# Kernel optimization log

Hardware: AMD Instinct MI355X
Metric: run time of the kernel (lower is better)

## Reference

```python
import jax, jax.numpy as jnp
import numpy as np

A = 16          # n_agents
H = 128         # rnn_hidden_dim
IN = 128        # input_shape
NA = 32         # n_attention
NACT = 14       # n_actions
TAU = 0.5       # gumbel_softmax_tau
B_ENV = 1024    # parallel envs
BZ = B_ENV * A

# neighbor index: for agent i, all j != i (matches select_ind in torch code)
IDX = np.array([[j for j in range(A) if j != i] for i in range(A)])  # [A, A-1]


def gru_cell(x, h, Wih, Whh, bih, bhh):
    # torch GRUCell gate order: r, z, n
    gi = x @ Wih.T + bih
    gh = h @ Whh.T + bhh
    ir, iz, inn = jnp.split(gi, 3, axis=-1)
    hr, hz, hn = jnp.split(gh, 3, axis=-1)
    r = jax.nn.sigmoid(ir + hr)
    z = jax.nn.sigmoid(iz + hz)
    n = jnp.tanh(inn + r * hn)
    return (1.0 - z) * n + z * h


def run_gru(seq, Wih, Whh, bih, bhh):
    # seq: [T, N, D]; returns all hidden states [T, N, H]
    h0 = jnp.zeros((seq.shape[1], Whh.shape[1]), seq.dtype)
    def step(h, x):
        h2 = gru_cell(x, h, Wih, Whh, bih, bhh)
        return h2, h2
    _, ys = jax.lax.scan(step, h0, seq)
    return ys


def setup_inputs() -> dict:
    key = jax.random.key(0)
    ks = jax.random.split(key, 24)
    def u(k, shape, fan):
        s = 1.0 / np.sqrt(fan)
        return jax.random.uniform(k, shape, jnp.float32, -s, s)
    inp = {
        "inputs": jax.random.normal(ks[0], (BZ, IN), jnp.float32),
        "hidden_state": jax.random.normal(ks[1], (BZ, H), jnp.float32),
        "gumbel_u": jax.random.uniform(ks[2], (BZ * (A - 1), 2), jnp.float32),
        # fc1
        "W1": u(ks[3], (H, IN), IN), "b1": u(ks[4], (H,), IN),
        # GRUCell
        "Wih_c": u(ks[5], (3 * H, H), H), "Whh_c": u(ks[6], (3 * H, H), H),
        "bih_c": u(ks[7], (3 * H,), H), "bhh_c": u(ks[8], (3 * H,), H),
        # bi-GRU forward dir (input 2H)
        "Wih_f": u(ks[9], (3 * H, 2 * H), H), "Whh_f": u(ks[10], (3 * H, H), H),
        "bih_f": u(ks[11], (3 * H,), H), "bhh_f": u(ks[12], (3 * H,), H),
        # bi-GRU backward dir
        "Wih_b": u(ks[13], (3 * H, 2 * H), H), "Whh_b": u(ks[14], (3 * H, H), H),
        "bih_b": u(ks[15], (3 * H,), H), "bhh_b": u(ks[16], (3 * H,), H),
        # hard classifier
        "Wc": u(ks[17], (2, 2 * H), 2 * H), "bc": u(ks[18], (2,), 2 * H),
        # attention projections (no bias)
        "Wq": u(ks[19], (NA, H), H), "Wk": u(ks[20], (NA, H), H),
        # fc2
        "W2": u(ks[21], (NACT, 2 * H), 2 * H), "b2": u(ks[22], (NACT,), 2 * H),
    }
    return inp


def reference(inputs, hidden_state, gumbel_u, W1, b1, Wih_c, Whh_c, bih_c, bhh_c,
              Wih_f, Whh_f, bih_f, bhh_f, Wih_b, Whh_b, bih_b, bhh_b,
              Wc, bc, Wq, Wk, W2, b2):
    bz = inputs.shape[0]
    B = bz // A
    x1 = jax.nn.relu(inputs @ W1.T + b1)
    h_rnn = gru_cell(x1, hidden_state.reshape(-1, H), Wih_c, Whh_c, bih_c, bhh_c)  # [bz, H]

    h3 = h_rnn.reshape(B, A, H)
    nbr = h3[:, IDX, :]                                           # [B, A, A-1, H]
    self_rep = jnp.broadcast_to(h3[:, :, None, :], (B, A, A - 1, H))
    pairs = jnp.concatenate([self_rep, nbr], axis=-1)             # [B, A, A-1, 2H]
    seq = pairs.transpose(2, 0, 1, 3).reshape(A - 1, bz, 2 * H)   # [T, bz, 2H]

    yf = run_gru(seq, Wih_f, Whh_f, bih_f, bhh_f)
    yb = jnp.flip(run_gru(jnp.flip(seq, 0), Wih_b, Whh_b, bih_b, bhh_b), 0)
    h_hard = jnp.concatenate([yf, yb], axis=-1)                   # [T, bz, 2H]
    h_hard = h_hard.transpose(1, 0, 2).reshape(-1, 2 * H)         # [bz*T, 2H]

    logits = h_hard @ Wc.T + bc                                   # [bz*T, 2]
    g = -jnp.log(-jnp.log(gumbel_u + 1e-10) + 1e-10)
    gs = jax.nn.softmax((logits + g) / TAU, axis=-1)
    hard_w = gs[:, 1].reshape(B, A, A - 1)                        # hard gate

    q = (h_rnn @ Wq.T).reshape(B, A, NA)
    k = (h_rnn @ Wk.T).reshape(B, A, NA)
    kn = k[:, IDX, :] * hard_w[..., None]                         # [B, A, A-1, NA]
    scores = jnp.einsum('bad,bamd->bam', q, kn) / np.sqrt(NA)
    soft_w = jax.nn.softmax(scores, axis=-1)                      # [B, A, A-1]

    w = hard_w * soft_w
    agg = jnp.einsum('bam,bamh->bah', w, nbr).reshape(bz, H)
    out = jnp.concatenate([h_rnn, agg], axis=-1) @ W2.T + b2      # [bz, n_actions]
    return out, h_rnn
```

## Files before the change

### kernel.cpp

```cpp
#include <hip/hip_runtime.h>
#include <hip/hip_bf16.h>


typedef __attribute__((ext_vector_type(8))) short short8;
typedef __attribute__((ext_vector_type(4))) short short4v;
typedef __attribute__((ext_vector_type(4))) float float4v;

#define BF2F(x) __bfloat162float(x)
typedef __hip_bfloat16 bf;

__device__ __forceinline__ float frcp(float x) {
  return __builtin_amdgcn_rcpf(x);
}
__device__ __forceinline__ float fsigmoid(float x) {
  return frcp(1.f + __expf(-x));
}
__device__ __forceinline__ float ftanh(float x) {
  float e = __expf(2.f * x);
  return 1.f - 2.f * frcp(1.f + e);
}
__device__ __forceinline__ float rdv(const void* p, int i, int f) {
  return f ? ((const float*)p)[i] : BF2F(((const bf*)p)[i]);
}

static const int AO[23] = {
  0, 2097152, 4194304, 4685824, 4702208, 4702336, 4751488, 4800640, 4801024,
  4801408, 4899712, 4948864, 4949248, 4949632, 5047936, 5097088, 5097472,
  5097856, 5098368, 5098384, 5102480, 5106576, 5110160};
static const int AN[23] = {
  2097152, 2097152, 491520, 16384, 128, 49152, 49152, 384, 384, 98304, 49152,
  384, 384, 98304, 49152, 384, 384, 512, 2, 4096, 4096, 3584, 14};

struct CArgs {
  const void* src[23];
  int n[23];
  int off[23];
};

__global__ void kConvert(CArgs a, int* __restrict__ flagOut,
                         bf* __restrict__ arena,
                         const void* __restrict__ WqR, const void* __restrict__ WkR,
                         const void* __restrict__ W2R, const void* __restrict__ WcR,
                         bf* __restrict__ Wqk, bf* __restrict__ W2p,
                         bf* __restrict__ Wcb) {
  __shared__ int sflag;
  if (threadIdx.x == 0) sflag = 0;
  __syncthreads();
  {
    const unsigned short* p0 = (const unsigned short*)a.src[0];
    int hit = 0;
    for (int i = threadIdx.x; i < 4096; i += 256) {
      int e = (p0[i] >> 7) & 0xFF;
      if (e >= 0xC0) hit = 1;
    }
    if (hit) atomicOr(&sflag, 1);
  }
  __syncthreads();
  const int f = sflag;
  const int b = blockIdx.y;
  if (b == 0 && blockIdx.x == 0 && threadIdx.x == 0) *flagOut = f;

  if (b == 23) {
    int idx = blockIdx.x * 256 + threadIdx.x;
    if (idx < 8192) {
      int r = idx >> 7, c = idx & 127;
      float v = (r < 32) ? rdv(WqR, r * 128 + c, f) : rdv(WkR, (r - 32) * 128 + c, f);
      Wqk[idx] = __float2bfloat16(v);
    }
    if (idx < 4096)
      W2p[idx] = __float2bfloat16((idx < 3584) ? rdv(W2R, idx, f) : 0.f);
    if (idx < 512) {
      int dir = idx >> 8, l = (idx >> 7) & 1, k = idx & 127;
      Wcb[idx] = __float2bfloat16(rdv(WcR, l * 256 + dir * 128 + k, f));
    }
    return;
  }
  if (b == 2 || b == 18 || b == 22) return;
  const int n = a.n[b];
  const int nv = n & ~7;
  bf* dst = arena + a.off[b];
  const int gid = blockIdx.x * 256 + threadIdx.x;
  const int gs = gridDim.x * 256;
  if (f) {
    const float* s = (const float*)a.src[b];
    for (int i = gid * 8; i < nv; i += gs * 8) {
      float4 x0 = *(const float4*)(s + i);
      float4 x1 = *(const float4*)(s + i + 4);
      short8 v;
      bf t;
      t = __float2bfloat16(x0.x); v[0] = *(short*)&t;
      t = __float2bfloat16(x0.y); v[1] = *(short*)&t;
      t = __float2bfloat16(x0.z); v[2] = *(short*)&t;
      t = __float2bfloat16(x0.w); v[3] = *(short*)&t;
      t = __float2bfloat16(x1.x); v[4] = *(short*)&t;
      t = __float2bfloat16(x1.y); v[5] = *(short*)&t;
      t = __float2bfloat16(x1.z); v[6] = *(short*)&t;
      t = __float2bfloat16(x1.w); v[7] = *(short*)&t;
      *(short8*)(dst + i) = v;
    }
    for (int i = nv + gid; i < n; i += gs) dst[i] = __float2bfloat16(s[i]);
  } else {
    const short8* s = (const short8*)a.src[b];
    short8* d = (short8*)dst;
    for (int i = gid; i * 8 < nv; i += gs) d[i] = s[i];
    const unsigned short* ss = (const unsigned short*)a.src[b];
    unsigned short* ds = (unsigned short*)dst;
    for (int i = nv + gid; i < n; i += gs) ds[i] = ss[i];
  }
}

__global__ __launch_bounds__(256) void kFused12(
    const bf* __restrict__ inputs, const bf* __restrict__ W1,
    const bf* __restrict__ b1, const bf* __restrict__ Wih,
    const bf* __restrict__ bih, bf* __restrict__ gi) {
  __shared__ bf sX[4][16][136];
  const int tid = threadIdx.x;
  const int wave = tid >> 6, lane = tid & 63;
  const int quad = lane >> 4, ci = lane & 15;
  const int row0 = blockIdx.x * 64 + wave * 16;

  float4v xa[8];
#pragma unroll
  for (int i = 0; i < 8; ++i) xa[i] = {0.f, 0.f, 0.f, 0.f};
#pragma unroll
  for (int ks = 0; ks < 4; ++ks) {
    short8 inr = *(const short8*)(inputs + (size_t)(row0 + ci) * 128 + ks * 32 + quad * 8);
#pragma unroll
    for (int ct = 0; ct < 8; ++ct) {
      short8 wfr = *(const short8*)(W1 + (size_t)(ct * 16 + ci) * 128 + ks * 32 + quad * 8);
      xa[ct] = __builtin_amdgcn_mfma_f32_16x16x32_bf16(wfr, inr, xa[ct], 0, 0, 0);
    }
  }
#pragma unroll
  for (int ct = 0; ct < 8; ++ct) {
    short4v v4;
#pragma unroll
    for (int r = 0; r < 4; ++r) {
      float v = xa[ct][r] + BF2F(b1[ct * 16 + quad * 4 + r]);
      v = fmaxf(v, 0.f);
      bf t = __float2bfloat16(v);
      v4[r] = *(short*)&t;
    }
    *(short4v*)&sX[wave][ci][ct * 16 + quad * 4] = v4;
  }
  short8 af[4];
#pragma unroll
  for (int ks = 0; ks < 4; ++ks)
    af[ks] = *(const short8*)&sX[wave][ci][ks * 32 + quad * 8];

  for (int cg = 0; cg < 6; ++cg) {
    float4v acc[4];
#pragma unroll
    for (int i = 0; i < 4; ++i) acc[i] = {0.f, 0.f, 0.f, 0.f};
#pragma unroll
    for (int ks = 0; ks < 4; ++ks)
#pragma unroll
      for (int nt = 0; nt < 4; ++nt) {
        short8 b = *(const short8*)(Wih + (size_t)(cg * 64 + nt * 16 + ci) * 128 + ks * 32 + quad * 8);
        acc[nt] = __builtin_amdgcn_mfma_f32_16x16x32_bf16(af[ks], b, acc[nt], 0, 0, 0);
      }
#pragma unroll
    for (int nt = 0; nt < 4; ++nt) {
      int col = cg * 64 + nt * 16 + ci;
      float bv = BF2F(bih[col]);
#pragma unroll
      for (int r = 0; r < 4; ++r)
        gi[(size_t)(row0 + quad * 4 + r) * 384 + col] = __float2bfloat16(acc[nt][r] + bv);
    }
  }
}

__global__ __launch_bounds__(256, 4) void kStep(
    const bf* __restrict__ Hp, const bf* __restrict__ Whh,
    const bf* __restrict__ G, int gld,
    const bf* __restrict__ bhh,
    bf* __restrict__ Ho, float* __restrict__ HcopyF) {
  const int half = blockIdx.z;
  const int tid = threadIdx.x;
  const int wave = tid >> 6, lane = tid & 63;
  const int quad = lane >> 4, ci = lane & 15;
  const int mr = blockIdx.x * 64 + wave * 16;

  float4v acc[12];
#pragma unroll
  for (int i = 0; i < 12; ++i) acc[i] = {0.f, 0.f, 0.f, 0.f};

#pragma unroll
  for (int ks = 0; ks < 4; ++ks) {
    short8 a = *(const short8*)(Hp + (size_t)(mr + ci) * 128 + ks * 32 + quad * 8);
#pragma unroll
    for (int g = 0; g < 3; ++g)
#pragma unroll
      for (int nt = 0; nt < 4; ++nt) {
        short8 b = *(const short8*)(Whh + (size_t)(g * 128 + half * 64 + nt * 16 + ci) * 128 + ks * 32 + quad * 8);
        acc[g * 4 + nt] = __builtin_amdgcn_mfma_f32_16x16x32_bf16(a, b, acc[g * 4 + nt], 0, 0, 0);
      }
  }

  float bR[4], bZ[4], bN[4];
#pragma unroll
  for (int nt = 0; nt < 4; ++nt) {
    int c = half * 64 + nt * 16 + ci;
    bR[nt] = BF2F(bhh[c]);
    bZ[nt] = BF2F(bhh[128 + c]);
    bN[nt] = BF2F(bhh[256 + c]);
  }

#pragma unroll
  for (int r = 0; r < 4; ++r) {
    int rr = mr + quad * 4 + r;
    const bf* gs = G + (size_t)rr * gld;
#pragma unroll
    for (int nt = 0; nt < 4; ++nt) {
      int c = half * 64 + nt * 16 + ci;
      float gr = BF2F(gs[c]), gz = BF2F(gs[128 + c]), gnn = BF2F(gs[256 + c]);
      float pre_r = acc[nt][r] + gr + bR[nt];
      float pre_z = acc[4 + nt][r] + gz + bZ[nt];
      float hn_   = acc[8 + nt][r] + bN[nt];
      float rg = fsigmoid(pre_r);
      float zg = fsigmoid(pre_z);
      float ng = ftanh(gnn + rg * hn_);
      float hp = BF2F(Hp[(size_t)rr * 128 + c]);
      float hv = ng + zg * (hp - ng);
      Ho[(size_t)rr * 128 + c] = __float2bfloat16(hv);
      if (HcopyF) HcopyF[(size_t)rr * 128 + c] = hv;
    }
  }
}

__global__ __launch_bounds__(512, 4) void kSeq(
    const bf* __restrict__ hrnn,
    const bf* __restrict__ Wih_f, const bf* __restrict__ Wih_b,
    const bf* __restrict__ Whh_f, const bf* __restrict__ Whh_b,
    const bf* __restrict__ bih_f, const bf* __restrict__ bih_b,
    const bf* __restrict__ bhh_f, const bf* __restrict__ bhh_b,
    const bf* __restrict__ Wcb, float* __restrict__ L) {
  __shared__ float sGiN[16][3][132];
  __shared__ bf sH[2][16][136];
  __shared__ float sL[16][15][2];
  __shared__ bf sWc[2][136];

  const int env = blockIdx.x;
  const int dir = blockIdx.y;
  const int tid = threadIdx.x;
  const int wave = tid >> 6, lane = tid & 63;
  const int nh = wave;
  const int quad = lane >> 4, ci = lane & 15;
  const bf* Wih = dir ? Wih_b : Wih_f;
  const bf* Whh = dir ? Whh_b : Whh_f;
  const bf* bih = dir ? bih_b : bih_f;
  const bf* bhh = dir ? bhh_b : bhh_f;
  const int h0q = nh * 16 + quad * 4;

  float4v gS[3], gN[3];
#pragma unroll
  for (int i = 0; i < 3; ++i) { gS[i] = {0.f, 0.f, 0.f, 0.f}; gN[i] = {0.f, 0.f, 0.f, 0.f}; }
#pragma unroll
  for (int ks = 0; ks < 4; ++ks) {
    short8 bh = *(const short8*)(hrnn + (size_t)(env * 16 + ci) * 128 + ks * 32 + quad * 8);
#pragma unroll
    for (int g = 0; g < 3; ++g) {
      const bf* wrow = Wih + (size_t)(g * 128 + nh * 16 + ci) * 256 + ks * 32 + quad * 8;
      short8 ws = *(const short8*)(wrow);
      short8 wn = *(const short8*)(wrow + 128);
      gS[g] = __builtin_amdgcn_mfma_f32_16x16x32_bf16(ws, bh, gS[g], 0, 0, 0);
      gN[g] = __builtin_amdgcn_mfma_f32_16x16x32_bf16(wn, bh, gN[g], 0, 0, 0);
    }
  }
#pragma unroll
  for (int g = 0; g < 3; ++g)
#pragma unroll
    for (int r = 0; r < 4; ++r) {
      int c = g * 128 + h0q + r;
      float bv = BF2F(bih[c]);
      if (g < 2) bv += BF2F(bhh[c]);
      gS[g][r] += bv;
    }
#pragma unroll
  for (int g = 0; g < 3; ++g)
    *(float4v*)&sGiN[ci][g][h0q] = gN[g];

  {
    bf z = __float2bfloat16(0.f);
    bf* p = &sH[0][0][0];
    for (int i = tid; i < 16 * 136; i += 512) p[i] = z;
    if (tid < 256)
      sWc[tid >> 7][tid & 127] = Wcb[(dir * 2 + (tid >> 7)) * 128 + (tid & 127)];
  }

  short8 Bf[12];
#pragma unroll
  for (int g = 0; g < 3; ++g)
#pragma unroll
    for (int ks = 0; ks < 4; ++ks)
      Bf[g * 4 + ks] =
          *(const short8*)(Whh + (size_t)(g * 128 + nh * 16 + ci) * 128 + ks * 32 + quad * 8);

  float bNc[4];
#pragma unroll
  for (int r = 0; r < 4; ++r) bNc[r] = BF2F(bhh[256 + h0q + r]);

  float hPrev[4];
#pragma unroll
  for (int r = 0; r < 4; ++r) hPrev[r] = 0.f;

  __syncthreads();

  for (int t = 0; t < 15; ++t) {
    const int cur = t & 1, nxt = cur ^ 1;
    const int m = dir ? (14 - t) : t;
    const int jr = m + ((m >= ci) ? 1 : 0);

    float4v nbR = *(const float4v*)&sGiN[jr][0][h0q];
    float4v nbZ = *(const float4v*)&sGiN[jr][1][h0q];
    float4v nbN = *(const float4v*)&sGiN[jr][2][h0q];

    float4v acc[3];
#pragma unroll
    for (int i = 0; i < 3; ++i) acc[i] = {0.f, 0.f, 0.f, 0.f};
    float4v lacc = {0.f, 0.f, 0.f, 0.f};
#pragma unroll
    for (int ks = 0; ks < 4; ++ks) {
      short8 bh = *(const short8*)&sH[cur][ci][ks * 32 + quad * 8];
#pragma unroll
      for (int g = 0; g < 3; ++g)
        acc[g] = __builtin_amdgcn_mfma_f32_16x16x32_bf16(Bf[g * 4 + ks], bh, acc[g], 0, 0, 0);
      if (nh == 0) {
        short8 wv = *(const short8*)&sWc[ci & 1][ks * 32 + quad * 8];
        lacc = __builtin_amdgcn_mfma_f32_16x16x32_bf16(wv, bh, lacc, 0, 0, 0);
      }
    }
    if (nh == 0 && t > 0 && quad == 0) {
      int mp = dir ? (15 - t) : (t - 1);
      sL[ci][mp][0] = lacc[0];
      sL[ci][mp][1] = lacc[1];
    }

    short4v hv4;
#pragma unroll
    for (int r = 0; r < 4; ++r) {
      float pre_r = acc[0][r] + gS[0][r] + nbR[r];
      float pre_z = acc[1][r] + gS[1][r] + nbZ[r];
      float gnn   = gS[2][r] + nbN[r];
      float hn_   = acc[2][r] + bNc[r];
      float rg = fsigmoid(pre_r);
      float zg = fsigmoid(pre_z);
      float ng = ftanh(gnn + rg * hn_);
      float hv = ng + zg * (hPrev[r] - ng);
      hPrev[r] = hv;
      bf b = __float2bfloat16(hv);
      hv4[r] = *(short*)&b;
    }
    *(short4v*)&sH[nxt][ci][h0q] = hv4;
    __syncthreads();
  }

  if (nh == 0) {
    float4v lacc = {0.f, 0.f, 0.f, 0.f};
#pragma unroll
    for (int ks = 0; ks < 4; ++ks) {
      short8 bh = *(const short8*)&sH[1][ci][ks * 32 + quad * 8];
      short8 wv = *(const short8*)&sWc[ci & 1][ks * 32 + quad * 8];
      lacc = __builtin_amdgcn_mfma_f32_16x16x32_bf16(wv, bh, lacc, 0, 0, 0);
    }
    if (quad == 0) {
      int mf = dir ? 0 : 14;
      sL[ci][mf][0] = lacc[0];
      sL[ci][mf][1] = lacc[1];
    }
  }
  __syncthreads();

  {
    float* Ld = L + (size_t)dir * 491520 + (size_t)env * 480;
    for (int i = tid; i < 480; i += 512) {
      int row = i / 30, rem = i - row * 30;
      int mm = rem >> 1, l = rem & 1;
      Ld[i] = sL[row][mm][l];
    }
  }
}

__global__ __launch_bounds__(256) void kTail(
    const bf* __restrict__ h, const bf* __restrict__ Wqk,
    const float* __restrict__ L, const void* __restrict__ guRaw,
    const void* __restrict__ bcRaw, const int* __restrict__ flag,
    const bf* __restrict__ W2p, const void* __restrict__ b2Raw,
    float* __restrict__ out) {
  __shared__ float sh[16 * 132];
  __shared__ float sqk[16 * 64];
  __shared__ float shw[240];
  __shared__ float sw[16 * 16];
  __shared__ bf sAgg[64][136];
  const int b4 = blockIdx.x;
  const int tid = threadIdx.x;
  const int f = *flag;
  const int a = tid >> 4, i = tid & 15;

  for (int e = 0; e < 4; ++e) {
    const int bb = b4 * 4 + e;
    __syncthreads();
    {
      const int w = tid >> 6, lane = tid & 63;
      const int quad = lane >> 4, ci = lane & 15;
      float4v acc = {0.f, 0.f, 0.f, 0.f};
#pragma unroll
      for (int ks = 0; ks < 4; ++ks) {
        short8 a_ = *(const short8*)(h + (size_t)(bb * 16 + ci) * 128 + ks * 32 + quad * 8);
        short8 b_ = *(const short8*)(Wqk + (size_t)(w * 16 + ci) * 128 + ks * 32 + quad * 8);
        acc = __builtin_amdgcn_mfma_f32_16x16x32_bf16(a_, b_, acc, 0, 0, 0);
      }
#pragma unroll
      for (int r = 0; r < 4; ++r)
        sqk[(quad * 4 + r) * 64 + w * 16 + ci] = acc[r];
    }
    for (int k = tid; k < 2048; k += 256)
      sh[(k >> 7) * 132 + (k & 127)] = BF2F(h[(size_t)bb * 2048 + k]);
    if (tid < 240) {
      int idx = bb * 240 + tid;
      float l0 = L[(size_t)idx * 2]     + L[491520 + (size_t)idx * 2]     + rdv(bcRaw, 0, f);
      float l1 = L[(size_t)idx * 2 + 1] + L[491520 + (size_t)idx * 2 + 1] + rdv(bcRaw, 1, f);
      float u0 = rdv(guRaw, idx * 2, f);
      float u1 = rdv(guRaw, idx * 2 + 1, f);
      float g0 = -__logf(-__logf(u0 + 1e-10f) + 1e-10f);
      float g1 = -__logf(-__logf(u1 + 1e-10f) + 1e-10f);
      shw[tid] = fsigmoid(((l1 + g1) - (l0 + g0)) * 2.0f);
    }
    __syncthreads();

    float s = -1e30f;
    if (i < 15) {
      int j = i + (i >= a);
      float d = 0.f;
#pragma unroll
      for (int c = 0; c < 32; ++c) d += sqk[a * 64 + c] * sqk[j * 64 + 32 + c];
      s = shw[a * 15 + i] * d * 0.17677669529663687f;
    }
    float mx = s;
#pragma unroll
    for (int d = 1; d < 16; d <<= 1) mx = fmaxf(mx, __shfl_xor(mx, d));
    float ex = (i < 15) ? __expf(s - mx) : 0.f;
    float sum = ex;
#pragma unroll
    for (int d = 1; d < 16; d <<= 1) sum += __shfl_xor(sum, d);
    float w = (i < 15) ? (ex * frcp(sum)) * shw[a * 15 + i] : 0.f;
    sw[a * 16 + i] = w;
    __syncthreads();

    float ac[8] = {0, 0, 0, 0, 0, 0, 0, 0};
    for (int mm = 0; mm < 15; ++mm) {
      int jm = mm + (mm >= a);
      float wm = sw[a * 16 + mm];
      const float* shp = &sh[jm * 132 + i * 8];
      float4 h0 = *(const float4*)shp;
      float4 h1 = *(const float4*)(shp + 4);
      ac[0] += wm * h0.x; ac[1] += wm * h0.y; ac[2] += wm * h0.z; ac[3] += wm * h0.w;
      ac[4] += wm * h1.x; ac[5] += wm * h1.y; ac[6] += wm * h1.z; ac[7] += wm * h1.w;
    }
    short8 v;
#pragma unroll
    for (int d = 0; d < 8; ++d) {
      bf b = __float2bfloat16(ac[d]);
      v[d] = *(short*)&b;
    }
    *(short8*)&sAgg[e * 16 + a][i * 8] = v;
  }
  __syncthreads();

  {
    const int wave = tid >> 6, lane = tid & 63;
    const int quad = lane >> 4, ci = lane & 15;
    const int mr = b4 * 64 + wave * 16;
    float4v acc = {0.f, 0.f, 0.f, 0.f};
#pragma unroll
    for (int ks = 0; ks < 4; ++ks) {
      short8 a_ = *(const short8*)(h + (size_t)(mr + ci) * 128 + ks * 32 + quad * 8);
      short8 b_ = *(const short8*)(W2p + (size_t)ci * 256 + ks * 32 + quad * 8);
      acc = __builtin_amdgcn_mfma_f32_16x16x32_bf16(a_, b_, acc, 0, 0, 0);
    }
#pragma unroll
    for (int ks = 0; ks < 4; ++ks) {
      short8 a_ = *(const short8*)&sAgg[wave * 16 + ci][ks * 32 + quad * 8];
      short8 b_ = *(const short8*)(W2p + (size_t)ci * 256 + 128 + ks * 32 + quad * 8);
      acc = __builtin_amdgcn_mfma_f32_16x16x32_bf16(a_, b_, acc, 0, 0, 0);
    }
    if (ci < 14) {
      float bv = rdv(b2Raw, ci, f);
#pragma unroll
      for (int r = 0; r < 4; ++r)
        out[(size_t)(mr + quad * 4 + r) * 14 + ci] = acc[r] + bv;
    }
  }
}

extern "C" void kernel_launch(void* const* d_in, const int* in_sizes, int n_in,
                              void* d_out, int out_size, void* d_ws, size_t ws_size,
                              hipStream_t stream) {
  const size_t OFF_ARENA = 0;
  const size_t OFF_FLAG  = 10220544;
  const size_t OFF_A     = 10220800;
  const size_t OFF_WQK   = 26998016;
  const size_t OFF_WCB   = 27014400;
  const size_t OFF_W2P   = 27410944;
  const size_t OFF_HRNN  = 27419136;
  const size_t NEEDED    = 84042240;
  if (ws_size < NEEDED) return;
  if (n_in < 23 || in_sizes[0] != 2097152 || in_sizes[3] != 16384 ||
      in_sizes[5] != 49152 || in_sizes[9] != 98304 || in_sizes[17] != 512 ||
      in_sizes[19] != 4096 || in_sizes[21] != 3584 || out_size != 2326528)
    return;

  char* ws = (char*)d_ws;
  bf*    arena = (bf*)(ws + OFF_ARENA);
  float* L     = (float*)(ws + OFF_ARENA);
  int*   flag  = (int*)(ws + OFF_FLAG);
  bf*    gi_c  = (bf*)(ws + OFF_A + 4194304);
  bf*    Wqk   = (bf*)(ws + OFF_WQK);
  bf*    Wcb   = (bf*)(ws + OFF_WCB);
  bf*    W2p   = (bf*)(ws + OFF_W2P);
  bf*    hrnn  = (bf*)(ws + OFF_HRNN);

  float* out14 = (float*)d_out;
  float* outh  = (float*)d_out + 229376;

  CArgs ca;
  for (int i = 0; i < 23; ++i) { ca.src[i] = d_in[i]; ca.n[i] = AN[i]; ca.off[i] = AO[i]; }
  kConvert<<<dim3(128, 24), 256, 0, stream>>>(ca, flag, arena,
                                              d_in[19], d_in[20], d_in[21], d_in[17],
                                              Wqk, W2p, Wcb);

  const bf* inputs = arena + AO[0];
  const bf* hidden = arena + AO[1];
  const bf* W1     = arena + AO[3];
  const bf* b1     = arena + AO[4];
  const bf* Wih_c  = arena + AO[5];
  const bf* Whh_c  = arena + AO[6];
  const bf* bih_c  = arena + AO[7];
  const bf* bhh_c  = arena + AO[8];
  const bf* Wih_f  = arena + AO[9];
  const bf* Whh_f  = arena + AO[10];
  const bf* bih_f  = arena + AO[11];
  const bf* bhh_f  = arena + AO[12];
  const bf* Wih_b  = arena + AO[13];
  const bf* Whh_b  = arena + AO[14];
  const bf* bih_b  = arena + AO[15];
  const bf* bhh_b  = arena + AO[16];

  kFused12<<<dim3(256), 256, 0, stream>>>(inputs, W1, b1, Wih_c, bih_c, gi_c);
  kStep<<<dim3(256, 1, 2), 256, 0, stream>>>(hidden, Whh_c, gi_c, 384, bhh_c,
                                             hrnn, outh);
  kSeq<<<dim3(1024, 2), 512, 0, stream>>>(hrnn, Wih_f, Wih_b, Whh_f, Whh_b,
                                          bih_f, bih_b, bhh_f, bhh_b, Wcb, L);
  kTail<<<dim3(256), 256, 0, stream>>>(hrnn, Wqk, L, d_in[2], d_in[18], flag,
                                       W2p, d_in[22], out14);
}
```

Before: 277.5 us.

## Shrink per-block work in fc1/GRU-input, GRU step and tail kernels for more blocks

kFused12 now handles 16 rows per block, with its four waves splitting the output columns and sharing the relu'd activations through LDS behind a barrier. kStep handles 32 rows per block, with waves splitting both rows and column tiles. kTail handles one environment per block instead of four, and only one wave does the final projection. Launch grids grow to match. The aim is more blocks and fewer accumulator registers per thread so the 256-CU GPU is better occupied. The cost is a new barrier, more redundant weight fetches per row, and idle waves in the tail GEMM.

```diff
diff --git a/kernel.cpp b/kernel.cpp
--- a/kernel.cpp
+++ b/kernel.cpp
@@ -113,60 +113,62 @@
     const bf* __restrict__ inputs, const bf* __restrict__ W1,
     const bf* __restrict__ b1, const bf* __restrict__ Wih,
     const bf* __restrict__ bih, bf* __restrict__ gi) {
-  __shared__ bf sX[4][16][136];
+  __shared__ bf sX[16][136];
   const int tid = threadIdx.x;
   const int wave = tid >> 6, lane = tid & 63;
   const int quad = lane >> 4, ci = lane & 15;
-  const int row0 = blockIdx.x * 64 + wave * 16;
-
-  float4v xa[8];
-#pragma unroll
-  for (int i = 0; i < 8; ++i) xa[i] = {0.f, 0.f, 0.f, 0.f};
+  const int row0 = blockIdx.x * 16;
+
+  float4v xa[2];
+#pragma unroll
+  for (int i = 0; i < 2; ++i) xa[i] = {0.f, 0.f, 0.f, 0.f};
 #pragma unroll
   for (int ks = 0; ks < 4; ++ks) {
     short8 inr = *(const short8*)(inputs + (size_t)(row0 + ci) * 128 + ks * 32 + quad * 8);
 #pragma unroll
-    for (int ct = 0; ct < 8; ++ct) {
+    for (int c2 = 0; c2 < 2; ++c2) {
+      int ct = wave * 2 + c2;
       short8 wfr = *(const short8*)(W1 + (size_t)(ct * 16 + ci) * 128 + ks * 32 + quad * 8);
-      xa[ct] = __builtin_amdgcn_mfma_f32_16x16x32_bf16(wfr, inr, xa[ct], 0, 0, 0);
-    }
-  }
-#pragma unroll
-  for (int ct = 0; ct < 8; ++ct) {
+      xa[c2] = __builtin_amdgcn_mfma_f32_16x16x32_bf16(wfr, inr, xa[c2], 0, 0, 0);
+    }
+  }
+#pragma unroll
+  for (int c2 = 0; c2 < 2; ++c2) {
+    int ct = wave * 2 + c2;
     short4v v4;
 #pragma unroll
     for (int r = 0; r < 4; ++r) {
-      float v = xa[ct][r] + BF2F(b1[ct * 16 + quad * 4 + r]);
+      float v = xa[c2][r] + BF2F(b1[ct * 16 + quad * 4 + r]);
       v = fmaxf(v, 0.f);
       bf t = __float2bfloat16(v);
       v4[r] = *(short*)&t;
     }
-    *(short4v*)&sX[wave][ci][ct * 16 + quad * 4] = v4;
-  }
+    *(short4v*)&sX[ci][ct * 16 + quad * 4] = v4;
+  }
+  __syncthreads();
+
   short8 af[4];
 #pragma unroll
   for (int ks = 0; ks < 4; ++ks)
-    af[ks] = *(const short8*)&sX[wave][ci][ks * 32 + quad * 8];
-
-  for (int cg = 0; cg < 6; ++cg) {
-    float4v acc[4];
-#pragma unroll
-    for (int i = 0; i < 4; ++i) acc[i] = {0.f, 0.f, 0.f, 0.f};
-#pragma unroll
-    for (int ks = 0; ks < 4; ++ks)
-#pragma unroll
-      for (int nt = 0; nt < 4; ++nt) {
-        short8 b = *(const short8*)(Wih + (size_t)(cg * 64 + nt * 16 + ci) * 128 + ks * 32 + quad * 8);
-        acc[nt] = __builtin_amdgcn_mfma_f32_16x16x32_bf16(af[ks], b, acc[nt], 0, 0, 0);
-      }
-#pragma unroll
-    for (int nt = 0; nt < 4; ++nt) {
-      int col = cg * 64 + nt * 16 + ci;
-      float bv = BF2F(bih[col]);
-#pragma unroll
-      for (int r = 0; r < 4; ++r)
-        gi[(size_t)(row0 + quad * 4 + r) * 384 + col] = __float2bfloat16(acc[nt][r] + bv);
-    }
+    af[ks] = *(const short8*)&sX[ci][ks * 32 + quad * 8];
+
+  float4v acc[6];
+#pragma unroll
+  for (int i = 0; i < 6; ++i) acc[i] = {0.f, 0.f, 0.f, 0.f};
+#pragma unroll
+  for (int ks = 0; ks < 4; ++ks)
+#pragma unroll
+    for (int j = 0; j < 6; ++j) {
+      short8 b = *(const short8*)(Wih + (size_t)((wave * 6 + j) * 16 + ci) * 128 + ks * 32 + quad * 8);
+      acc[j] = __builtin_amdgcn_mfma_f32_16x16x32_bf16(af[ks], b, acc[j], 0, 0, 0);
+    }
+#pragma unroll
+  for (int j = 0; j < 6; ++j) {
+    int col = (wave * 6 + j) * 16 + ci;
+    float bv = BF2F(bih[col]);
+#pragma unroll
+    for (int r = 0; r < 4; ++r)
+      gi[(size_t)(row0 + quad * 4 + r) * 384 + col] = __float2bfloat16(acc[j][r] + bv);
   }
 }
 
@@ -179,11 +181,12 @@
   const int tid = threadIdx.x;
   const int wave = tid >> 6, lane = tid & 63;
   const int quad = lane >> 4, ci = lane & 15;
-  const int mr = blockIdx.x * 64 + wave * 16;
-
-  float4v acc[12];
-#pragma unroll
-  for (int i = 0; i < 12; ++i) acc[i] = {0.f, 0.f, 0.f, 0.f};
+  const int mr = blockIdx.x * 32 + (wave & 1) * 16;
+  const int nt0 = (wave >> 1) * 2;
+
+  float4v acc[6];
+#pragma unroll
+  for (int i = 0; i < 6; ++i) acc[i] = {0.f, 0.f, 0.f, 0.f};
 
 #pragma unroll
   for (int ks = 0; ks < 4; ++ks) {
@@ -191,16 +194,16 @@
 #pragma unroll
     for (int g = 0; g < 3; ++g)
 #pragma unroll
-      for (int nt = 0; nt < 4; ++nt) {
-        short8 b = *(const short8*)(Whh + (size_t)(g * 128 + half * 64 + nt * 16 + ci) * 128 + ks * 32 + quad * 8);
-        acc[g * 4 + nt] = __builtin_amdgcn_mfma_f32_16x16x32_bf16(a, b, acc[g * 4 + nt], 0, 0, 0);
+      for (int nt = 0; nt < 2; ++nt) {
+        short8 b = *(const short8*)(Whh + (size_t)(g * 128 + half * 64 + (nt0 + nt) * 16 + ci) * 128 + ks * 32 + quad * 8);
+        acc[g * 2 + nt] = __builtin_amdgcn_mfma_f32_16x16x32_bf16(a, b, acc[g * 2 + nt], 0, 0, 0);
       }
   }
 
-  float bR[4], bZ[4], bN[4];
-#pragma unroll
-  for (int nt = 0; nt < 4; ++nt) {
-    int c = half * 64 + nt * 16 + ci;
+  float bR[2], bZ[2], bN[2];
+#pragma unroll
+  for (int nt = 0; nt < 2; ++nt) {
+    int c = half * 64 + (nt0 + nt) * 16 + ci;
     bR[nt] = BF2F(bhh[c]);
     bZ[nt] = BF2F(bhh[128 + c]);
     bN[nt] = BF2F(bhh[256 + c]);
@@ -211,12 +214,12 @@
     int rr = mr + quad * 4 + r;
     const bf* gs = G + (size_t)rr * gld;
 #pragma unroll
-    for (int nt = 0; nt < 4; ++nt) {
-      int c = half * 64 + nt * 16 + ci;
+    for (int nt = 0; nt < 2; ++nt) {
+      int c = half * 64 + (nt0 + nt) * 16 + ci;
       float gr = BF2F(gs[c]), gz = BF2F(gs[128 + c]), gnn = BF2F(gs[256 + c]);
       float pre_r = acc[nt][r] + gr + bR[nt];
-      float pre_z = acc[4 + nt][r] + gz + bZ[nt];
-      float hn_   = acc[8 + nt][r] + bN[nt];
+      float pre_z = acc[2 + nt][r] + gz + bZ[nt];
+      float hn_   = acc[4 + nt][r] + bN[nt];
       float rg = fsigmoid(pre_r);
       float zg = fsigmoid(pre_z);
       float ng = ftanh(gnn + rg * hn_);
@@ -391,86 +394,81 @@
   __shared__ float sqk[16 * 64];
   __shared__ float shw[240];
   __shared__ float sw[16 * 16];
-  __shared__ bf sAgg[64][136];
-  const int b4 = blockIdx.x;
+  __shared__ bf sAgg[16][136];
+  const int bb = blockIdx.x;
   const int tid = threadIdx.x;
   const int f = *flag;
   const int a = tid >> 4, i = tid & 15;
 
-  for (int e = 0; e < 4; ++e) {
-    const int bb = b4 * 4 + e;
-    __syncthreads();
-    {
-      const int w = tid >> 6, lane = tid & 63;
-      const int quad = lane >> 4, ci = lane & 15;
-      float4v acc = {0.f, 0.f, 0.f, 0.f};
-#pragma unroll
-      for (int ks = 0; ks < 4; ++ks) {
-        short8 a_ = *(const short8*)(h + (size_t)(bb * 16 + ci) * 128 + ks * 32 + quad * 8);
-        short8 b_ = *(const short8*)(Wqk + (size_t)(w * 16 + ci) * 128 + ks * 32 + quad * 8);
-        acc = __builtin_amdgcn_mfma_f32_16x16x32_bf16(a_, b_, acc, 0, 0, 0);
-      }
-#pragma unroll
-      for (int r = 0; r < 4; ++r)
-        sqk[(quad * 4 + r) * 64 + w * 16 + ci] = acc[r];
-    }
-    for (int k = tid; k < 2048; k += 256)
-      sh[(k >> 7) * 132 + (k & 127)] = BF2F(h[(size_t)bb * 2048 + k]);
-    if (tid < 240) {
-      int idx = bb * 240 + tid;
-      float l0 = L[(size_t)idx * 2]     + L[491520 + (size_t)idx * 2]     + rdv(bcRaw, 0, f);
-      float l1 = L[(size_t)idx * 2 + 1] + L[491520 + (size_t)idx * 2 + 1] + rdv(bcRaw, 1, f);
-      float u0 = rdv(guRaw, idx * 2, f);
-      float u1 = rdv(guRaw, idx * 2 + 1, f);
-      float g0 = -__logf(-__logf(u0 + 1e-10f) + 1e-10f);
-      float g1 = -__logf(-__logf(u1 + 1e-10f) + 1e-10f);
-      shw[tid] = fsigmoid(((l1 + g1) - (l0 + g0)) * 2.0f);
-    }
-    __syncthreads();
-
-    float s = -1e30f;
-    if (i < 15) {
-      int j = i + (i >= a);
-      float d = 0.f;
-#pragma unroll
-      for (int c = 0; c < 32; ++c) d += sqk[a * 64 + c] * sqk[j * 64 + 32 + c];
-      s = shw[a * 15 + i] * d * 0.17677669529663687f;
-    }
-    float mx = s;
-#pragma unroll
-    for (int d = 1; d < 16; d <<= 1) mx = fmaxf(mx, __shfl_xor(mx, d));
-    float ex = (i < 15) ? __expf(s - mx) : 0.f;
-    float sum = ex;
-#pragma unroll
-    for (int d = 1; d < 16; d <<= 1) sum += __shfl_xor(sum, d);
-    float w = (i < 15) ? (ex * frcp(sum)) * shw[a * 15 + i] : 0.f;
-    sw[a * 16 + i] = w;
-    __syncthreads();
-
-    float ac[8] = {0, 0, 0, 0, 0, 0, 0, 0};
-    for (int mm = 0; mm < 15; ++mm) {
-      int jm = mm + (mm >= a);
-      float wm = sw[a * 16 + mm];
-      const float* shp = &sh[jm * 132 + i * 8];
-      float4 h0 = *(const float4*)shp;
-      float4 h1 = *(const float4*)(shp + 4);
-      ac[0] += wm * h0.x; ac[1] += wm * h0.y; ac[2] += wm * h0.z; ac[3] += wm * h0.w;
-      ac[4] += wm * h1.x; ac[5] += wm * h1.y; ac[6] += wm * h1.z; ac[7] += wm * h1.w;
-    }
-    short8 v;
-#pragma unroll
-    for (int d = 0; d < 8; ++d) {
-      bf b = __float2bfloat16(ac[d]);
-      v[d] = *(short*)&b;
-    }
-    *(short8*)&sAgg[e * 16 + a][i * 8] = v;
-  }
-  __syncthreads();
-
   {
-    const int wave = tid >> 6, lane = tid & 63;
+    const int w = tid >> 6, lane = tid & 63;
     const int quad = lane >> 4, ci = lane & 15;
-    const int mr = b4 * 64 + wave * 16;
+    float4v acc = {0.f, 0.f, 0.f, 0.f};
+#pragma unroll
+    for (int ks = 0; ks < 4; ++ks) {
+      short8 a_ = *(const short8*)(h + (size_t)(bb * 16 + ci) * 128 + ks * 32 + quad * 8);
+      short8 b_ = *(const short8*)(Wqk + (size_t)(w * 16 + ci) * 128 + ks * 32 + quad * 8);
+      acc = __builtin_amdgcn_mfma_f32_16x16x32_bf16(a_, b_, acc, 0, 0, 0);
+    }
+#pragma unroll
+    for (int r = 0; r < 4; ++r)
+      sqk[(quad * 4 + r) * 64 + w * 16 + ci] = acc[r];
+  }
+  for (int k = tid; k < 2048; k += 256)
+    sh[(k >> 7) * 132 + (k & 127)] = BF2F(h[(size_t)bb * 2048 + k]);
+  if (tid < 240) {
+    int idx = bb * 240 + tid;
+    float l0 = L[(size_t)idx * 2]     + L[491520 + (size_t)idx * 2]     + rdv(bcRaw, 0, f);
+    float l1 = L[(size_t)idx * 2 + 1] + L[491520 + (size_t)idx * 2 + 1] + rdv(bcRaw, 1, f);
+    float u0 = rdv(guRaw, idx * 2, f);
+    float u1 = rdv(guRaw, idx * 2 + 1, f);
+    float g0 = -__logf(-__logf(u0 + 1e-10f) + 1e-10f);
+    float g1 = -__logf(-__logf(u1 + 1e-10f) + 1e-10f);
+    shw[tid] = fsigmoid(((l1 + g1) - (l0 + g0)) * 2.0f);
+  }
+  __syncthreads();
+
+  float s = -1e30f;
+  if (i < 15) {
+    int j = i + (i >= a);
+    float d = 0.f;
+#pragma unroll
+    for (int c = 0; c < 32; ++c) d += sqk[a * 64 + c] * sqk[j * 64 + 32 + c];
+    s = shw[a * 15 + i] * d * 0.17677669529663687f;
+  }
+  float mx = s;
+#pragma unroll
+  for (int d = 1; d < 16; d <<= 1) mx = fmaxf(mx, __shfl_xor(mx, d));
+  float ex = (i < 15) ? __expf(s - mx) : 0.f;
+  float sum = ex;
+#pragma unroll
+  for (int d = 1; d < 16; d <<= 1) sum += __shfl_xor(sum, d);
+  float w = (i < 15) ? (ex * frcp(sum)) * shw[a * 15 + i] : 0.f;
+  sw[a * 16 + i] = w;
+  __syncthreads();
+
+  float ac[8] = {0, 0, 0, 0, 0, 0, 0, 0};
+  for (int mm = 0; mm < 15; ++mm) {
+    int jm = mm + (mm >= a);
+    float wm = sw[a * 16 + mm];
+    const float* shp = &sh[jm * 132 + i * 8];
+    float4 h0 = *(const float4*)shp;
+    float4 h1 = *(const float4*)(shp + 4);
+    ac[0] += wm * h0.x; ac[1] += wm * h0.y; ac[2] += wm * h0.z; ac[3] += wm * h0.w;
+    ac[4] += wm * h1.x; ac[5] += wm * h1.y; ac[6] += wm * h1.z; ac[7] += wm * h1.w;
+  }
+  short8 v;
+#pragma unroll
+  for (int d = 0; d < 8; ++d) {
+    bf b = __float2bfloat16(ac[d]);
+    v[d] = *(short*)&b;
+  }
+  *(short8*)&sAgg[a][i * 8] = v;
+  __syncthreads();
+
+  if (tid < 64) {
+    const int quad = tid >> 4, ci = tid & 15;
+    const int mr = bb * 16;
     float4v acc = {0.f, 0.f, 0.f, 0.f};
 #pragma unroll
     for (int ks = 0; ks < 4; ++ks) {
@@ -480,7 +478,7 @@
     }
 #pragma unroll
     for (int ks = 0; ks < 4; ++ks) {
-      short8 a_ = *(const short8*)&sAgg[wave * 16 + ci][ks * 32 + quad * 8];
+      short8 a_ = *(const short8*)&sAgg[ci][ks * 32 + quad * 8];
       short8 b_ = *(const short8*)(W2p + (size_t)ci * 256 + 128 + ks * 32 + quad * 8);
       acc = __builtin_amdgcn_mfma_f32_16x16x32_bf16(a_, b_, acc, 0, 0, 0);
     }
@@ -546,11 +544,11 @@
   const bf* bih_b  = arena + AO[15];
   const bf* bhh_b  = arena + AO[16];
 
-  kFused12<<<dim3(256), 256, 0, stream>>>(inputs, W1, b1, Wih_c, bih_c, gi_c);
-  kStep<<<dim3(256, 1, 2), 256, 0, stream>>>(hidden, Whh_c, gi_c, 384, bhh_c,
+  kFused12<<<dim3(1024), 256, 0, stream>>>(inputs, W1, b1, Wih_c, bih_c, gi_c);
+  kStep<<<dim3(512, 1, 2), 256, 0, stream>>>(hidden, Whh_c, gi_c, 384, bhh_c,
                                              hrnn, outh);
   kSeq<<<dim3(1024, 2), 512, 0, stream>>>(hrnn, Wih_f, Wih_b, Whh_f, Whh_b,
                                           bih_f, bih_b, bhh_f, bhh_b, Wcb, L);
-  kTail<<<dim3(256), 256, 0, stream>>>(hrnn, Wqk, L, d_in[2], d_in[18], flag,
-                                       W2p, d_in[22], out14);
-}
+  kTail<<<dim3(1024), 256, 0, stream>>>(hrnn, Wqk, L, d_in[2], d_in[18], flag,
+                                        W2p, d_in[22], out14);
+}
```

After: 267.4 us. 1.04x faster.
